# Performance work log

Measured on AMD Instinct MI355X. Metric: run time of the kernel, lower is better.

The kernel has to match this reference:

```python
import jax, jax.numpy as jnp
import numpy as np

N_NODES = 50000
N_EDGES = 800000
HID = 64
N_GRAPHS = 64


def setup_inputs() -> dict:
    key = jax.random.key(0)
    ks = jax.random.split(key, 12)
    x = jax.random.normal(ks[0], (N_NODES, 1), dtype=jnp.float32)
    edge_index = jax.random.randint(ks[1], (2, N_EDGES), 0, N_NODES, dtype=jnp.int64)
    batch = jnp.sort(jax.random.randint(ks[2], (N_NODES,), 0, N_GRAPHS, dtype=jnp.int64))
    def glorot(k, shape):
        fan_in, fan_out = shape
        s = jnp.sqrt(2.0 / (fan_in + fan_out)).astype(jnp.float32)
        return jax.random.normal(k, shape, dtype=jnp.float32) * s
    return {
        "x": x, "edge_index": edge_index, "batch": batch,
        "W1l": glorot(ks[3], (1, HID)), "b1": jnp.zeros((HID,), jnp.float32), "W1r": glorot(ks[4], (1, HID)),
        "W2l": glorot(ks[5], (HID, HID)), "b2": jnp.zeros((HID,), jnp.float32), "W2r": glorot(ks[6], (HID, HID)),
        "W3l": glorot(ks[7], (HID, HID)), "b3": jnp.zeros((HID,), jnp.float32), "W3r": glorot(ks[8], (HID, HID)),
        "Wfc1": glorot(ks[9], (HID, HID // 2)), "bfc1": jnp.zeros((HID // 2,), jnp.float32),
        "Wfc2": glorot(ks[10], (HID // 2, 1)), "bfc2": jnp.zeros((1,), jnp.float32),
    }


def _sage_conv(x, src, dst, Wl, bl, Wr):
    # PyG SAGEConv (mean aggr): lin_l(mean_{j in N(i)} x_j) + lin_r(x_i)
    msgs = x[src]                                                   # [E, d] gather
    agg = jax.ops.segment_sum(msgs, dst, num_segments=N_NODES)      # [N, d] scatter-add
    cnt = jax.ops.segment_sum(jnp.ones((src.shape[0], 1), x.dtype), dst, num_segments=N_NODES)
    mean = agg / jnp.maximum(cnt, 1.0)                              # isolated nodes -> 0
    return mean @ Wl + bl + x @ Wr


def reference(x, edge_index, batch,
              W1l, b1, W1r, W2l, b2, W2r, W3l, b3, W3r,
              Wfc1, bfc1, Wfc2, bfc2):
    src, dst = edge_index[0], edge_index[1]
    layers = [(W1l, b1, W1r), (W2l, b2, W2r), (W3l, b3, W3r)]
    h = x
    for (Wl, bl, Wr) in layers:
        h_res = h
        h = jax.nn.relu(_sage_conv(h, src, dst, Wl, bl, Wr))
        # dropout is identity at inference; residual broadcasts [N,64]+[N,1] on layer 1
        h = h + h_res
    # global mean pool over graphs in the batch
    sums = jax.ops.segment_sum(h, batch, num_segments=N_GRAPHS)     # [G, d]
    cnts = jax.ops.segment_sum(jnp.ones((h.shape[0], 1), h.dtype), batch, num_segments=N_GRAPHS)
    pooled = sums / jnp.maximum(cnts, 1.0)
    out = jax.nn.relu(pooled @ Wfc1 + bfc1)
    out = out @ Wfc2 + bfc2                                          # [G, 1]
    return out
```

## Files before the change

### kernel.cpp

```cpp
#include <hip/hip_runtime.h>
#include <hip/hip_bf16.h>
#include <hip/hip_fp16.h>

#define HID 64
#define NGRAPHS 64
#define BUCKET 64
#define CAP 4096
#define EPB 2048
#define NSLOT 33

typedef _Float16 half8 __attribute__((ext_vector_type(8)));
typedef float floatx4 __attribute__((ext_vector_type(4)));
typedef float floatx2 __attribute__((ext_vector_type(2)));

__device__ __forceinline__ unsigned char enc_fp8(float v) {
    int pk = __builtin_amdgcn_cvt_pk_fp8_f32(v, v, 0, false);
    return (unsigned char)(pk & 0xff);
}

__global__ __launch_bounds__(256) void detect_init_kernel(const void* edge, const void* batch,
                                                          int* flags, int* bcursor,
                                                          float* psum,
                                                          const float* W2l, const float* W2r,
                                                          const float* W3l, const float* W3r,
                                                          __half* wl2h, __half* wr2h,
                                                          __half* wl3h, __half* wr3h,
                                                          int E2, int N, int G, int NB) {
    int t = threadIdx.x;
    int b = blockIdx.x;
    if (b == 0) {
        for (int i = t; i < NB; i += 256) bcursor[i] = i * CAP;
        for (int i = t; i < G * HID; i += 256) psum[i] = 0.0f;
        if (t < 64) {
            int lane = t;
            int half_ = E2 / 2;
            int stride = half_ / 64; if (stride < 1) stride = 1;
            int j = lane * stride; if (j >= half_) j = half_ - 1;
            long long v = ((const long long*)edge)[j];
            bool ok = (v >= 0 && v < (long long)N);
            unsigned long long m = __ballot(ok);
            if (lane == 0) flags[0] = (m == ~0ULL) ? 1 : 0;
            int halfB = N / 2;
            int strideB = halfB / 64; if (strideB < 1) strideB = 1;
            int jb = lane * strideB; if (jb >= halfB) jb = halfB - 1;
            long long vb = ((const long long*)batch)[jb];
            bool okb = (vb >= 0 && vb < (long long)G);
            unsigned long long mb = __ballot(okb);
            if (lane == 0) flags[1] = (mb == ~0ULL) ? 1 : 0;
        }
    } else {
        const float* src = (b == 1) ? W2l : (b == 2) ? W2r : (b == 3) ? W3l : W3r;
        __half* dst = (b == 1) ? wl2h : (b == 2) ? wr2h : (b == 3) ? wl3h : wr3h;
        for (int i = t; i < HID * HID; i += 256) dst[i] = __float2half(src[i]);
    }
}

__device__ __forceinline__ int idx_at(const void* p, int i, bool is64) {
    return is64 ? (int)((const long long*)p)[i] : ((const int*)p)[i];
}

__global__ __launch_bounds__(256) void bin_scatter_kernel(const void* edge, const int* __restrict__ flags,
                                                          int* __restrict__ bcursor,
                                                          unsigned int* __restrict__ entries,
                                                          int E, int NB) {
    extern __shared__ int lds[];
    int* hist = lds;
    int* base = lds + NB;
    int* ssrc = lds + 2 * NB;
    int* sdst = ssrc + EPB;
    for (int i = threadIdx.x; i < NB; i += 256) hist[i] = 0;
    __syncthreads();
    bool is64 = flags[0] != 0;
    int start = blockIdx.x * EPB;
    int end = start + EPB; if (end > E) end = E;
    int cnt = end - start;
    for (int k = threadIdx.x; k < cnt; k += 256) {
        int e = start + k;
        int srcv = idx_at(edge, e, is64);
        int d = idx_at(edge, E + e, is64);
        ssrc[k] = srcv;
        sdst[k] = d;
        atomicAdd(&hist[d >> 6], 1);
    }
    __syncthreads();
    for (int i = threadIdx.x; i < NB; i += 256) {
        int h = hist[i];
        base[i] = h ? atomicAdd(&bcursor[i], h) : 0;
    }
    __syncthreads();
    for (int i = threadIdx.x; i < NB; i += 256) hist[i] = 0;
    __syncthreads();
    for (int k = threadIdx.x; k < cnt; k += 256) {
        int d = sdst[k];
        int b = d >> 6;
        int lo = atomicAdd(&hist[b], 1);
        int p = base[b] + lo;
        if (p < (b + 1) * CAP)
            entries[p] = ((unsigned int)ssrc[k] << 6) | (unsigned int)(d & 63);
    }
}

__global__ __launch_bounds__(256) void csr_l1_kernel(const unsigned int* __restrict__ entries,
                                                     const int* __restrict__ bcursor,
                                                     const float* __restrict__ x,
                                                     const float* __restrict__ W1l,
                                                     const float* __restrict__ b1,
                                                     const float* __restrict__ W1r,
                                                     int* __restrict__ rowptr,
                                                     int* __restrict__ deg,
                                                     int* __restrict__ csr,
                                                     __half* __restrict__ h1h,
                                                     unsigned char* __restrict__ h1q,
                                                     int N, int NB) {
    __shared__ int hist[BUCKET];
    __shared__ int lstart[BUCKET];
    __shared__ int lcur[BUCKET];
    __shared__ float accx[BUCKET];
    __shared__ float sx[BUCKET];
    int t = threadIdx.x;
    int b = blockIdx.x;
    int r0 = b * CAP;
    int cnt = bcursor[b] - r0; if (cnt > CAP) cnt = CAP;
    if (t < BUCKET) {
        hist[t] = 0; lcur[t] = 0; accx[t] = 0.0f;
        int node = b * BUCKET + t;
        sx[t] = (node < N) ? x[node] : 0.0f;
    }
    __syncthreads();
    for (int j = r0 + t; j < r0 + cnt; j += 256) {
        unsigned int en = entries[j];
        atomicAdd(&hist[en & 63u], 1);
        atomicAdd(&accx[en & 63u], x[en >> 6]);
    }
    __syncthreads();
    if (t < BUCKET) {
        int v = hist[t];
        int s = v;
#pragma unroll
        for (int off = 1; off < 64; off <<= 1) {
            int u = __shfl_up(s, off);
            if (t >= off) s += u;
        }
        lstart[t] = s - v;
        int node = b * BUCKET + t;
        if (node < N) {
            rowptr[node] = r0 + s - v;
            deg[node] = v;
        }
    }
    __syncthreads();
    for (int j = r0 + t; j < r0 + cnt; j += 256) {
        unsigned int en = entries[j];
        int dl = (int)(en & 63u);
        int p = atomicAdd(&lcur[dl], 1);
        csr[r0 + lstart[dl] + p] = (int)(en >> 6);
    }
    __syncthreads();
    int f = t & 63;
    int sub = t >> 6;
    float wlf = W1l[f], bf = b1[f], wrf = W1r[f];
    for (int it = 0; it < 16; ++it) {
        int nl = it * 4 + sub;
        int node = b * BUCKET + nl;
        if (node < N) {
            int d = hist[nl];
            float mv = (d > 0) ? accx[nl] / (float)d : 0.0f;
            float xv = sx[nl];
            float v = fmaf(mv, wlf, fmaf(xv, wrf, bf));
            v = v > 0.0f ? v : 0.0f;
            float hv = v + xv;
            h1h[(size_t)node * HID + f] = __float2half(hv);
            h1q[(size_t)node * HID + f] = enc_fp8(hv);
        }
    }
}

__global__ __launch_bounds__(256) void gather_mfma_kernel(const int* __restrict__ rowptr,
                                                          const int* __restrict__ deg,
                                                          const int* __restrict__ csr,
                                                          const unsigned char* __restrict__ hq,
                                                          const __half* __restrict__ hph,
                                                          const __half* __restrict__ Wlh,
                                                          const float* __restrict__ bvec,
                                                          const __half* __restrict__ Wrh,
                                                          __half* __restrict__ houth,
                                                          unsigned char* __restrict__ houtq,
                                                          float* __restrict__ psum,
                                                          const void* batch,
                                                          const int* __restrict__ flags,
                                                          int N) {
    __shared__ _Float16 smean[32][HID + 8];
    __shared__ float spool[NSLOT][HID];
    __shared__ int sb[32];
    int t = threadIdx.x;
    bool pool = (psum != nullptr);
    if (pool) {
        for (int i = t; i < NSLOT * HID; i += 256) ((float*)spool)[i] = 0.0f;
        if (t < 32) {
            int node = blockIdx.x * 32 + t;
            sb[t] = (node < N) ? idx_at(batch, node, flags[1] != 0) : -1;
        }
    }

    {
        int grp = t >> 3;
        int l = t & 7;
        int i = blockIdx.x * 32 + grp;
        if (i < N) {
            int r0 = rowptr[i];
            int d = deg[i];
            int r1 = r0 + d;
            float a[4][8];
#pragma unroll
            for (int w = 0; w < 4; ++w)
#pragma unroll
                for (int k = 0; k < 8; ++k) a[w][k] = 0.0f;
            int j = r0;
            for (; j + 8 <= r1; j += 8) {
                uint2 u[8];
#pragma unroll
                for (int m = 0; m < 8; ++m) {
                    int s = csr[j + m];
                    u[m] = *(const uint2*)(hq + (size_t)s * HID + l * 8);
                }
#pragma unroll
                for (int m = 0; m < 8; ++m) {
                    floatx2 p0 = __builtin_amdgcn_cvt_pk_f32_fp8(u[m].x, false);
                    floatx2 p1 = __builtin_amdgcn_cvt_pk_f32_fp8(u[m].x, true);
                    floatx2 p2 = __builtin_amdgcn_cvt_pk_f32_fp8(u[m].y, false);
                    floatx2 p3 = __builtin_amdgcn_cvt_pk_f32_fp8(u[m].y, true);
                    int w = m & 3;
                    a[w][0] += p0[0]; a[w][1] += p0[1];
                    a[w][2] += p1[0]; a[w][3] += p1[1];
                    a[w][4] += p2[0]; a[w][5] += p2[1];
                    a[w][6] += p3[0]; a[w][7] += p3[1];
                }
            }
            for (; j < r1; ++j) {
                int s = csr[j];
                uint2 u0 = *(const uint2*)(hq + (size_t)s * HID + l * 8);
                floatx2 p0 = __builtin_amdgcn_cvt_pk_f32_fp8(u0.x, false);
                floatx2 p1 = __builtin_amdgcn_cvt_pk_f32_fp8(u0.x, true);
                floatx2 p2 = __builtin_amdgcn_cvt_pk_f32_fp8(u0.y, false);
                floatx2 p3 = __builtin_amdgcn_cvt_pk_f32_fp8(u0.y, true);
                a[0][0] += p0[0]; a[0][1] += p0[1];
                a[0][2] += p1[0]; a[0][3] += p1[1];
                a[0][4] += p2[0]; a[0][5] += p2[1];
                a[0][6] += p3[0]; a[0][7] += p3[1];
            }
            float inv = (d > 0) ? 1.0f / (float)d : 0.0f;
            __half2 o[4];
#pragma unroll
            for (int q = 0; q < 4; ++q) {
                float lo = ((a[0][2*q]   + a[1][2*q])   + (a[2][2*q]   + a[3][2*q]))   * inv;
                float hi = ((a[0][2*q+1] + a[1][2*q+1]) + (a[2][2*q+1] + a[3][2*q+1])) * inv;
                o[q] = __floats2half2_rn(lo, hi);
            }
            *(uint4*)&smean[grp][l * 8] = *(uint4*)o;
        }
    }
    __syncthreads();

    int wave = t >> 6;
    int lane = t & 63;
    int m = lane & 15;
    int quad = lane >> 4;
    int node0 = blockIdx.x * 32 + wave * 16;
    if (wave < 2 && node0 < N) {
        const _Float16* wlp = (const _Float16*)Wlh;
        const _Float16* wrp = (const _Float16*)Wrh;
        half8 bl[2][4], br[2][4];
#pragma unroll
        for (int kh = 0; kh < 2; ++kh)
#pragma unroll
            for (int nt = 0; nt < 4; ++nt) {
                half8 vl, vr;
#pragma unroll
                for (int j = 0; j < 8; ++j) {
                    int k = kh * 32 + quad * 8 + j;
                    vl[j] = wlp[k * HID + nt * 16 + m];
                    vr[j] = wrp[k * HID + nt * 16 + m];
                }
                bl[kh][nt] = vl;
                br[kh][nt] = vr;
            }
        int nlA = wave * 16 + m;
        half8 am0 = *(const half8*)&smean[nlA][quad * 8];
        half8 am1 = *(const half8*)&smean[nlA][32 + quad * 8];
        int nodeA = node0 + m; if (nodeA >= N) nodeA = N - 1;
        const _Float16* hrow = (const _Float16*)hph + (size_t)nodeA * HID;
        half8 ah0 = *(const half8*)(hrow + quad * 8);
        half8 ah1 = *(const half8*)(hrow + 32 + quad * 8);

#pragma unroll
        for (int nt = 0; nt < 4; ++nt) {
            float b = bvec[nt * 16 + m];
            floatx4 c = {b, b, b, b};
            c = __builtin_amdgcn_mfma_f32_16x16x32_f16(am0, bl[0][nt], c, 0, 0, 0);
            c = __builtin_amdgcn_mfma_f32_16x16x32_f16(am1, bl[1][nt], c, 0, 0, 0);
            c = __builtin_amdgcn_mfma_f32_16x16x32_f16(ah0, br[0][nt], c, 0, 0, 0);
            c = __builtin_amdgcn_mfma_f32_16x16x32_f16(ah1, br[1][nt], c, 0, 0, 0);
            int f = nt * 16 + m;
#pragma unroll
            for (int r = 0; r < 4; ++r) {
                int nodeR = node0 + quad * 4 + r;
                if (nodeR < N) {
                    float v = c[r];
                    v = v > 0.0f ? v : 0.0f;
                    v += __half2float(((const __half*)hph)[(size_t)nodeR * HID + f]);
                    if (!pool) {
                        houth[(size_t)nodeR * HID + f] = __float2half(v);
                        houtq[(size_t)nodeR * HID + f] = enc_fp8(v);
                    } else {
                        int bg = sb[wave * 16 + quad * 4 + r];
                        int slot = bg - sb[0];
                        if (slot < NSLOT) atomicAdd(&spool[slot][f], v);
                        else atomicAdd(&psum[bg * HID + f], v);
                    }
                }
            }
        }
    }

    if (pool) {
        __syncthreads();
        int gbase = sb[0];
        for (int i = t; i < NSLOT * HID; i += 256) {
            int s = i >> 6, f = i & 63;
            float v = spool[s][f];
            if (v != 0.0f) atomicAdd(&psum[(gbase + s) * HID + f], v);
        }
    }
}

__device__ __forceinline__ int lbound(const void* batch, int n, long long key, bool is64) {
    int lo = 0, hi = n;
    while (lo < hi) {
        int mid = (lo + hi) >> 1;
        long long v = is64 ? ((const long long*)batch)[mid] : (long long)((const int*)batch)[mid];
        if (v < key) lo = mid + 1; else hi = mid;
    }
    return lo;
}

__global__ __launch_bounds__(64) void fc_kernel(const float* __restrict__ psum,
                                                const void* batch,
                                                const int* __restrict__ flags,
                                                const float* __restrict__ Wfc1,
                                                const float* __restrict__ bfc1,
                                                const float* __restrict__ Wfc2,
                                                const float* __restrict__ bfc2,
                                                float* __restrict__ out, int N) {
    __shared__ int sb2[2];
    __shared__ float mean[HID];
    int g = blockIdx.x;
    int t = threadIdx.x;
    bool is64 = flags[1] != 0;
    if (t == 0) sb2[0] = lbound(batch, N, g, is64);
    if (t == 1) sb2[1] = lbound(batch, N, g + 1, is64);
    __syncthreads();
    float c = fmaxf((float)(sb2[1] - sb2[0]), 1.0f);
    mean[t] = psum[g * HID + t] / c;
    __syncthreads();
    float v = 0.0f;
    if (t < 32) {
        float acc = bfc1[t];
#pragma unroll
        for (int k = 0; k < HID; ++k) acc += mean[k] * Wfc1[k * 32 + t];
        float hcc = acc > 0.0f ? acc : 0.0f;
        v = hcc * Wfc2[t];
    }
#pragma unroll
    for (int off = 32; off >= 1; off >>= 1) v += __shfl_down(v, off);
    if (t == 0) out[g] = v + bfc2[0];
}

extern "C" void kernel_launch(void* const* d_in, const int* in_sizes, int n_in,
                              void* d_out, int out_size, void* d_ws, size_t ws_size,
                              hipStream_t stream) {
    const int N = in_sizes[0];
    const int E2 = in_sizes[1];
    const int E = E2 / 2;
    const int NB = (N + BUCKET - 1) / BUCKET;

    const float* x    = (const float*)d_in[0];
    const void*  edge = d_in[1];
    const void*  batch= d_in[2];
    const float* W1l  = (const float*)d_in[3];
    const float* b1   = (const float*)d_in[4];
    const float* W1r  = (const float*)d_in[5];
    const float* W2l  = (const float*)d_in[6];
    const float* b2   = (const float*)d_in[7];
    const float* W2r  = (const float*)d_in[8];
    const float* W3l  = (const float*)d_in[9];
    const float* b3   = (const float*)d_in[10];
    const float* W3r  = (const float*)d_in[11];
    const float* Wfc1 = (const float*)d_in[12];
    const float* bfc1 = (const float*)d_in[13];
    const float* Wfc2 = (const float*)d_in[14];
    const float* bfc2 = (const float*)d_in[15];
    float* out = (float*)d_out;

    char* ws = (char*)d_ws;
    size_t o = 0;
    auto alloc = [&](size_t bytes) { char* p = ws + o; o += (bytes + 255) & ~(size_t)255; return p; };
    int*   bcursor = (int*)alloc((size_t)NB * 4);
    float* psum    = (float*)alloc((size_t)NGRAPHS * HID * 4);
    unsigned int* entries = (unsigned int*)alloc((size_t)NB * CAP * 4);
    int*   csr     = (int*)alloc((size_t)NB * CAP * 4);
    int*   rowptr  = (int*)alloc((size_t)N * 4);
    int*   deg     = (int*)alloc((size_t)N * 4);
    __half* h1h    = (__half*)alloc((size_t)N * HID * 2);
    __half* h2h    = (__half*)alloc((size_t)N * HID * 2);
    unsigned char* h1q = (unsigned char*)alloc((size_t)N * HID);
    unsigned char* h2q = (unsigned char*)alloc((size_t)N * HID);
    __half* wl2h   = (__half*)alloc((size_t)HID * HID * 2);
    __half* wr2h   = (__half*)alloc((size_t)HID * HID * 2);
    __half* wl3h   = (__half*)alloc((size_t)HID * HID * 2);
    __half* wr3h   = (__half*)alloc((size_t)HID * HID * 2);
    int*   flags   = (int*)alloc(16);

    detect_init_kernel<<<5, 256, 0, stream>>>(edge, batch, flags, bcursor, psum,
                                              W2l, W2r, W3l, W3r, wl2h, wr2h, wl3h, wr3h,
                                              E2, N, NGRAPHS, NB);

    const int nblk = (E + EPB - 1) / EPB;
    const int scatter_lds = (2 * NB + 2 * EPB) * 4;
    bin_scatter_kernel<<<nblk, 256, scatter_lds, stream>>>(edge, flags, bcursor, entries, E, NB);

    csr_l1_kernel<<<NB, 256, 0, stream>>>(entries, bcursor, x, W1l, b1, W1r,
                                          rowptr, deg, csr, h1h, h1q, N, NB);

    const int fusedBlocks = (N + 31) / 32;

    gather_mfma_kernel<<<fusedBlocks, 256, 0, stream>>>(rowptr, deg, csr, h1q, h1h,
                                                        wl2h, b2, wr2h, h2h, h2q,
                                                        (float*)nullptr, nullptr, flags, N);

    gather_mfma_kernel<<<fusedBlocks, 256, 0, stream>>>(rowptr, deg, csr, h2q, h2h,
                                                        wl3h, b3, wr3h, (__half*)nullptr,
                                                        (unsigned char*)nullptr,
                                                        psum, batch, flags, N);

    fc_kernel<<<NGRAPHS, 64, 0, stream>>>(psum, batch, flags, Wfc1, bfc1, Wfc2, bfc2, out, N);
}
```

Before: 209.2 us.

## Process 64 nodes per block with 16-byte gathers and prepacked MFMA weight fragments

The fused gather+MFMA kernel now assigns 4 threads per node (16-byte uint4 FP8 loads) instead of 8 (8-byte loads), so each block covers 64 nodes and all four waves run the MFMA epilogue instead of two. Layer weights are prepacked in the init kernel into the per-lane MFMA B-fragment order, so each lane loads a contiguous half8 instead of eight strided scalar loads. Fewer, wider gather loads and full wave use in the matmul stage target the memory-bound aggregation and the epilogue overhead. The cost is fewer threads per node, more registers per thread for accumulators, and half as many blocks.

```diff
diff --git a/kernel.cpp b/kernel.cpp
--- a/kernel.cpp
+++ b/kernel.cpp
@@ -18,13 +18,25 @@
     return (unsigned char)(pk & 0xff);
 }
 
+__device__ __forceinline__ void cvt_acc16(float* bank, const uint4& u) {
+    floatx2 p;
+    p = __builtin_amdgcn_cvt_pk_f32_fp8(u.x, false); bank[0] += p[0];  bank[1] += p[1];
+    p = __builtin_amdgcn_cvt_pk_f32_fp8(u.x, true);  bank[2] += p[0];  bank[3] += p[1];
+    p = __builtin_amdgcn_cvt_pk_f32_fp8(u.y, false); bank[4] += p[0];  bank[5] += p[1];
+    p = __builtin_amdgcn_cvt_pk_f32_fp8(u.y, true);  bank[6] += p[0];  bank[7] += p[1];
+    p = __builtin_amdgcn_cvt_pk_f32_fp8(u.z, false); bank[8] += p[0];  bank[9] += p[1];
+    p = __builtin_amdgcn_cvt_pk_f32_fp8(u.z, true);  bank[10] += p[0]; bank[11] += p[1];
+    p = __builtin_amdgcn_cvt_pk_f32_fp8(u.w, false); bank[12] += p[0]; bank[13] += p[1];
+    p = __builtin_amdgcn_cvt_pk_f32_fp8(u.w, true);  bank[14] += p[0]; bank[15] += p[1];
+}
+
 __global__ __launch_bounds__(256) void detect_init_kernel(const void* edge, const void* batch,
                                                           int* flags, int* bcursor,
                                                           float* psum,
                                                           const float* W2l, const float* W2r,
                                                           const float* W3l, const float* W3r,
-                                                          __half* wl2h, __half* wr2h,
-                                                          __half* wl3h, __half* wr3h,
+                                                          __half* wl2f, __half* wr2f,
+                                                          __half* wl3f, __half* wr3f,
                                                           int E2, int N, int G, int NB) {
     int t = threadIdx.x;
     int b = blockIdx.x;
@@ -50,8 +62,16 @@
         }
     } else {
         const float* src = (b == 1) ? W2l : (b == 2) ? W2r : (b == 3) ? W3l : W3r;
-        __half* dst = (b == 1) ? wl2h : (b == 2) ? wr2h : (b == 3) ? wl3h : wr3h;
-        for (int i = t; i < HID * HID; i += 256) dst[i] = __float2half(src[i]);
+        __half* dst = (b == 1) ? wl2f : (b == 2) ? wr2f : (b == 3) ? wl3f : wr3f;
+        for (int i = t; i < HID * HID; i += 256) {
+            int j = i & 7;
+            int lane = (i >> 3) & 63;
+            int nt = (i >> 9) & 3;
+            int kh = i >> 11;
+            int k = kh * 32 + (lane >> 4) * 8 + j;
+            int col = nt * 16 + (lane & 15);
+            dst[i] = __float2half(src[k * HID + col]);
+        }
     }
 }
 
@@ -180,83 +200,64 @@
                                                           const int* __restrict__ csr,
                                                           const unsigned char* __restrict__ hq,
                                                           const __half* __restrict__ hph,
-                                                          const __half* __restrict__ Wlh,
+                                                          const __half* __restrict__ Wlf,
                                                           const float* __restrict__ bvec,
-                                                          const __half* __restrict__ Wrh,
+                                                          const __half* __restrict__ Wrf,
                                                           __half* __restrict__ houth,
                                                           unsigned char* __restrict__ houtq,
                                                           float* __restrict__ psum,
                                                           const void* batch,
                                                           const int* __restrict__ flags,
                                                           int N) {
-    __shared__ _Float16 smean[32][HID + 8];
+    __shared__ _Float16 smean[64][HID + 8];
     __shared__ float spool[NSLOT][HID];
-    __shared__ int sb[32];
+    __shared__ int sb[64];
     int t = threadIdx.x;
     bool pool = (psum != nullptr);
     if (pool) {
         for (int i = t; i < NSLOT * HID; i += 256) ((float*)spool)[i] = 0.0f;
-        if (t < 32) {
-            int node = blockIdx.x * 32 + t;
+        if (t < 64) {
+            int node = blockIdx.x * 64 + t;
             sb[t] = (node < N) ? idx_at(batch, node, flags[1] != 0) : -1;
         }
     }
 
     {
-        int grp = t >> 3;
-        int l = t & 7;
-        int i = blockIdx.x * 32 + grp;
+        int grp = t >> 2;
+        int l = t & 3;
+        int i = blockIdx.x * 64 + grp;
         if (i < N) {
             int r0 = rowptr[i];
             int d = deg[i];
             int r1 = r0 + d;
-            float a[4][8];
-#pragma unroll
-            for (int w = 0; w < 4; ++w)
-#pragma unroll
-                for (int k = 0; k < 8; ++k) a[w][k] = 0.0f;
+            float a0[16], a1[16];
+#pragma unroll
+            for (int k = 0; k < 16; ++k) { a0[k] = 0.0f; a1[k] = 0.0f; }
             int j = r0;
             for (; j + 8 <= r1; j += 8) {
-                uint2 u[8];
+                uint4 u[8];
 #pragma unroll
                 for (int m = 0; m < 8; ++m) {
                     int s = csr[j + m];
-                    u[m] = *(const uint2*)(hq + (size_t)s * HID + l * 8);
+                    u[m] = *(const uint4*)(hq + (size_t)s * HID + l * 16);
                 }
 #pragma unroll
-                for (int m = 0; m < 8; ++m) {
-                    floatx2 p0 = __builtin_amdgcn_cvt_pk_f32_fp8(u[m].x, false);
-                    floatx2 p1 = __builtin_amdgcn_cvt_pk_f32_fp8(u[m].x, true);
-                    floatx2 p2 = __builtin_amdgcn_cvt_pk_f32_fp8(u[m].y, false);
-                    floatx2 p3 = __builtin_amdgcn_cvt_pk_f32_fp8(u[m].y, true);
-                    int w = m & 3;
-                    a[w][0] += p0[0]; a[w][1] += p0[1];
-                    a[w][2] += p1[0]; a[w][3] += p1[1];
-                    a[w][4] += p2[0]; a[w][5] += p2[1];
-                    a[w][6] += p3[0]; a[w][7] += p3[1];
-                }
+                for (int m = 0; m < 8; ++m) cvt_acc16((m & 1) ? a1 : a0, u[m]);
             }
             for (; j < r1; ++j) {
                 int s = csr[j];
-                uint2 u0 = *(const uint2*)(hq + (size_t)s * HID + l * 8);
-                floatx2 p0 = __builtin_amdgcn_cvt_pk_f32_fp8(u0.x, false);
-                floatx2 p1 = __builtin_amdgcn_cvt_pk_f32_fp8(u0.x, true);
-                floatx2 p2 = __builtin_amdgcn_cvt_pk_f32_fp8(u0.y, false);
-                floatx2 p3 = __builtin_amdgcn_cvt_pk_f32_fp8(u0.y, true);
-                a[0][0] += p0[0]; a[0][1] += p0[1];
-                a[0][2] += p1[0]; a[0][3] += p1[1];
-                a[0][4] += p2[0]; a[0][5] += p2[1];
-                a[0][6] += p3[0]; a[0][7] += p3[1];
+                uint4 u0 = *(const uint4*)(hq + (size_t)s * HID + l * 16);
+                cvt_acc16(a0, u0);
             }
             float inv = (d > 0) ? 1.0f / (float)d : 0.0f;
-            __half2 o[4];
-#pragma unroll
-            for (int q = 0; q < 4; ++q) {
-                float lo = ((a[0][2*q]   + a[1][2*q])   + (a[2][2*q]   + a[3][2*q]))   * inv;
-                float hi = ((a[0][2*q+1] + a[1][2*q+1]) + (a[2][2*q+1] + a[3][2*q+1])) * inv;
-                o[q] = __floats2half2_rn(lo, hi);
-            }
-            *(uint4*)&smean[grp][l * 8] = *(uint4*)o;
+            __half2 o[8];
+#pragma unroll
+            for (int q = 0; q < 8; ++q)
+                o[q] = __floats2half2_rn((a0[2 * q] + a1[2 * q]) * inv,
+                                         (a0[2 * q + 1] + a1[2 * q + 1]) * inv);
+            uint4* dst = (uint4*)&smean[grp][l * 16];
+            dst[0] = ((uint4*)o)[0];
+            dst[1] = ((uint4*)o)[1];
         }
     }
     __syncthreads();
@@ -265,24 +266,18 @@
     int lane = t & 63;
     int m = lane & 15;
     int quad = lane >> 4;
-    int node0 = blockIdx.x * 32 + wave * 16;
-    if (wave < 2 && node0 < N) {
-        const _Float16* wlp = (const _Float16*)Wlh;
-        const _Float16* wrp = (const _Float16*)Wrh;
+    int node0 = blockIdx.x * 64 + wave * 16;
+    if (node0 < N) {
+        const _Float16* wlp = (const _Float16*)Wlf;
+        const _Float16* wrp = (const _Float16*)Wrf;
         half8 bl[2][4], br[2][4];
 #pragma unroll
         for (int kh = 0; kh < 2; ++kh)
 #pragma unroll
             for (int nt = 0; nt < 4; ++nt) {
-                half8 vl, vr;
-#pragma unroll
-                for (int j = 0; j < 8; ++j) {
-                    int k = kh * 32 + quad * 8 + j;
-                    vl[j] = wlp[k * HID + nt * 16 + m];
-                    vr[j] = wrp[k * HID + nt * 16 + m];
-                }
-                bl[kh][nt] = vl;
-                br[kh][nt] = vr;
+                size_t off = (size_t)((kh * 4 + nt) * 64 + lane) * 8;
+                bl[kh][nt] = *(const half8*)(wlp + off);
+                br[kh][nt] = *(const half8*)(wrp + off);
             }
         int nlA = wave * 16 + m;
         half8 am0 = *(const half8*)&smean[nlA][quad * 8];
@@ -414,14 +409,14 @@
     __half* h2h    = (__half*)alloc((size_t)N * HID * 2);
     unsigned char* h1q = (unsigned char*)alloc((size_t)N * HID);
     unsigned char* h2q = (unsigned char*)alloc((size_t)N * HID);
-    __half* wl2h   = (__half*)alloc((size_t)HID * HID * 2);
-    __half* wr2h   = (__half*)alloc((size_t)HID * HID * 2);
-    __half* wl3h   = (__half*)alloc((size_t)HID * HID * 2);
-    __half* wr3h   = (__half*)alloc((size_t)HID * HID * 2);
+    __half* wl2f   = (__half*)alloc((size_t)HID * HID * 2);
+    __half* wr2f   = (__half*)alloc((size_t)HID * HID * 2);
+    __half* wl3f   = (__half*)alloc((size_t)HID * HID * 2);
+    __half* wr3f   = (__half*)alloc((size_t)HID * HID * 2);
     int*   flags   = (int*)alloc(16);
 
     detect_init_kernel<<<5, 256, 0, stream>>>(edge, batch, flags, bcursor, psum,
-                                              W2l, W2r, W3l, W3r, wl2h, wr2h, wl3h, wr3h,
+                                              W2l, W2r, W3l, W3r, wl2f, wr2f, wl3f, wr3f,
                                               E2, N, NGRAPHS, NB);
 
     const int nblk = (E + EPB - 1) / EPB;
@@ -431,14 +426,14 @@
     csr_l1_kernel<<<NB, 256, 0, stream>>>(entries, bcursor, x, W1l, b1, W1r,
                                           rowptr, deg, csr, h1h, h1q, N, NB);
 
-    const int fusedBlocks = (N + 31) / 32;
+    const int fusedBlocks = (N + 63) / 64;
 
     gather_mfma_kernel<<<fusedBlocks, 256, 0, stream>>>(rowptr, deg, csr, h1q, h1h,
-                                                        wl2h, b2, wr2h, h2h, h2q,
+                                                        wl2f, b2, wr2f, h2h, h2q,
                                                         (float*)nullptr, nullptr, flags, N);
 
     gather_mfma_kernel<<<fusedBlocks, 256, 0, stream>>>(rowptr, deg, csr, h2q, h2h,
-                                                        wl3h, b3, wr3h, (__half*)nullptr,
+                                                        wl3f, b3, wr3f, (__half*)nullptr,
                                                         (unsigned char*)nullptr,
                                                         psum, batch, flags, N);
 
```

New measurement: 203.0 us. -3.0%, faster.
